# Kernel optimization log

Measured on AMD Instinct MI355X. Metric: run time of the kernel, lower is better.

## Reference

```python
import jax, jax.numpy as jnp
import numpy as np

N_NODES = 2_000_000
N_EDGES = 32_000_000
N_GRAPHS = 256


def setup_inputs() -> dict:
    key = jax.random.key(0)
    k1, k2, k3 = jax.random.split(key, 3)
    probs = jax.random.uniform(k1, (N_NODES,), dtype=jnp.float32)
    edge_index = jax.random.randint(k2, (2, N_EDGES), 0, N_NODES, dtype=jnp.int64)
    batch = jnp.sort(jax.random.randint(k3, (N_NODES,), 0, N_GRAPHS, dtype=jnp.int64))
    penalty_coefficient = jnp.float32(0.25)
    return {
        "probs": probs,
        "edge_index": edge_index,
        "batch": batch,
        "penalty_coefficient": penalty_coefficient,
    }


def reference(probs, edge_index, batch, penalty_coefficient):
    # num_graphs = batch.max() + 1 (concrete; batch is a static index array)
    num_graphs = int(np.asarray(batch).max()) + 1

    row, col = edge_index[0], edge_index[1]
    # remove_self_loops: drop edges with row == col -> mask instead of filter (static shapes)
    not_self_loop = (row != col).astype(probs.dtype)

    # expected distance: sum over non-self-loop edges of (1 - p_u)(1 - p_v), / num_graphs
    vertex_row = probs[row]  # [E]
    vertex_col = probs[col]  # [E]
    expected_distance = jnp.sum((1.0 - vertex_row) * (1.0 - vertex_col) * not_self_loop) / num_graphs

    # per-graph sum of probs (the original's python loop over graphs == segment_sum)
    probs_sum = jax.ops.segment_sum(probs, batch, num_segments=num_graphs)  # [G]
    expected_weight = probs_sum.mean()

    loss = penalty_coefficient * expected_distance + expected_weight
    return jnp.stack([loss, expected_weight, expected_distance])
```

## Files before the change

### kernel.cpp

```cpp
#include <hip/hip_runtime.h>
#include <hip/hip_fp16.h>

#define THREADS 256

typedef int int4v __attribute__((ext_vector_type(4)));


__device__ __forceinline__ float h2f_bits(unsigned v) {
    __half_raw hr;
    hr.x = (unsigned short)v;
    return __half2float((__half)hr);
}

__device__ __forceinline__ void block_reduce_atomic(float local, double* dst,
                                                    double* sdata) {
    double d = (double)local;
    #pragma unroll
    for (int off = 32; off > 0; off >>= 1)
        d += __shfl_down(d, off, 64);
    int lane = threadIdx.x & 63;
    int wid  = threadIdx.x >> 6;
    if (lane == 0) sdata[wid] = d;
    __syncthreads();
    if (threadIdx.x == 0) {
        double s = 0.0;
        #pragma unroll
        for (int i = 0; i < (THREADS / 64); ++i) s += sdata[i];
        atomicAdd(dst, s);
    }
}

__global__ void __launch_bounds__(THREADS) build_table_kernel(
        const float* __restrict__ probs,
        unsigned short* __restrict__ qt,
        double* __restrict__ ws,
        long long n_nodes) {
    __shared__ double sdata[THREADS / 64];
    long long n4 = n_nodes >> 2;
    const float4* p4 = (const float4*)probs;
    ushort4* q4 = (ushort4*)qt;
    long long tid = (long long)blockIdx.x * blockDim.x + threadIdx.x;
    long long stride = (long long)gridDim.x * blockDim.x;

    if (tid == 0) qt[n_nodes] = (unsigned short)0;

    float local = 0.0f;
    for (long long i = tid; i < n4; i += stride) {
        float4 v = p4[i];
        local += (v.x + v.y) + (v.z + v.w);
        ushort4 q;
        q.x = __half_as_ushort(__float2half(1.0f - v.x));
        q.y = __half_as_ushort(__float2half(1.0f - v.y));
        q.z = __half_as_ushort(__float2half(1.0f - v.z));
        q.w = __half_as_ushort(__float2half(1.0f - v.w));
        q4[i] = q;
    }
    for (long long i = (n4 << 2) + tid; i < n_nodes; i += stride) {
        float p = probs[i];
        local += p;
        qt[i] = __half_as_ushort(__float2half(1.0f - p));
    }

    block_reduce_atomic(local, ws + 1, sdata);
}

__global__ void edge_sum_kernel(
        const unsigned short* __restrict__ qt,
        const int* __restrict__ row,
        const int* __restrict__ col,
        double* __restrict__ ws,
        long long n_edges,
        int sentinel) {
    __shared__ double sdata[THREADS / 64];
    long long n4 = n_edges >> 2;
    long long G4 = n4 >> 2;
    long long t  = (long long)blockIdx.x * blockDim.x + threadIdx.x;

    const int4v* row4 = (const int4v*)row;
    const int4v* col4 = (const int4v*)col;

    float local = 0.0f;
    if (t < G4) {
        unsigned av[16], bv[16];
        #pragma unroll
        for (int k = 0; k < 4; ++k) {
            int4v u = __builtin_nontemporal_load(&row4[t + (long long)k * G4]);
            int4v v = __builtin_nontemporal_load(&col4[t + (long long)k * G4]);
            int v0 = (u.x == v.x) ? sentinel : v.x;
            int v1 = (u.y == v.y) ? sentinel : v.y;
            int v2 = (u.z == v.z) ? sentinel : v.z;
            int v3 = (u.w == v.w) ? sentinel : v.w;
            av[4 * k + 0] = qt[u.x];
            av[4 * k + 1] = qt[u.y];
            av[4 * k + 2] = qt[u.z];
            av[4 * k + 3] = qt[u.w];
            bv[4 * k + 0] = qt[v0];
            bv[4 * k + 1] = qt[v1];
            bv[4 * k + 2] = qt[v2];
            bv[4 * k + 3] = qt[v3];
        }

        #pragma unroll
        for (int i = 0; i < 16; ++i)
            local += h2f_bits(av[i]) * h2f_bits(bv[i]);
    }

    long long covered = G4 << 4;
    long long total_threads = (long long)gridDim.x * blockDim.x;
    for (long long e = covered + t; e < n_edges; e += total_threads) {
        int uu = row[e], vv = col[e];
        int vr = (uu == vv) ? sentinel : vv;
        local += h2f_bits(qt[uu]) * h2f_bits(qt[vr]);
    }

    block_reduce_atomic(local, ws, sdata);
}

__global__ void finalize_kernel(const double* __restrict__ ws,
                                const int* __restrict__ batch,
                                long long n_nodes,
                                const float* __restrict__ pc,
                                float* __restrict__ out) {
    double edge_s = ws[0];
    double prob_s = ws[1];
    double G = (double)(batch[n_nodes - 1] + 1);
    double ed = edge_s / G;
    double ew = prob_s / G;
    double loss = (double)pc[0] * ed + ew;
    out[0] = (float)loss;
    out[1] = (float)ew;
    out[2] = (float)ed;
}

extern "C" void kernel_launch(void* const* d_in, const int* in_sizes, int n_in,
                              void* d_out, int out_size, void* d_ws, size_t ws_size,
                              hipStream_t stream) {
    const float* probs = (const float*)d_in[0];
    const int* edge_index = (const int*)d_in[1];
    const int* batch = (const int*)d_in[2];
    const float* pc = (const float*)d_in[3];

    long long n_nodes = (long long)in_sizes[0];
    long long n_edges = (long long)in_sizes[1] / 2;
    const int* row = edge_index;
    const int* col = edge_index + n_edges;

    double* ws = (double*)d_ws;
    hipMemsetAsync(ws, 0, 2 * sizeof(double), stream);

    unsigned short* qt = (unsigned short*)((char*)d_ws + 256);
    build_table_kernel<<<512, THREADS, 0, stream>>>(probs, qt, ws, n_nodes);

    long long T = (n_edges >> 2) >> 2;
    long long blocks = (T + THREADS - 1) / THREADS;
    if (blocks < 1) blocks = 1;
    edge_sum_kernel<<<(int)blocks, THREADS, 0, stream>>>(qt, row, col, ws,
                                                         n_edges, (int)n_nodes);

    finalize_kernel<<<1, 1, 0, stream>>>(ws, batch, n_nodes, pc, (float*)d_out);
}
```

Measured before the change: 319.0 us.

## Use one int4 edge chunk per thread with nontemporal inline-asm gathers

The edge kernel now gives each thread one 4-edge chunk instead of sixteen edges, which launches four times as many blocks. The half-precision table gathers are issued as inline-asm global_load_ushort with the nt cache hint, followed by an explicit waitcnt and a scheduling barrier. The intent is more parallelism for latency hiding and less cache pollution from the gathers. In exchange, the random gathers into the 4MB table may lose cache reuse, and more blocks mean more block reductions and double-precision atomics.

```diff
diff --git a/kernel.cpp b/kernel.cpp
--- a/kernel.cpp
+++ b/kernel.cpp
@@ -73,39 +73,51 @@
         int sentinel) {
     __shared__ double sdata[THREADS / 64];
     long long n4 = n_edges >> 2;
-    long long G4 = n4 >> 2;
     long long t  = (long long)blockIdx.x * blockDim.x + threadIdx.x;
 
     const int4v* row4 = (const int4v*)row;
     const int4v* col4 = (const int4v*)col;
 
     float local = 0.0f;
-    if (t < G4) {
-        unsigned av[16], bv[16];
-        #pragma unroll
-        for (int k = 0; k < 4; ++k) {
-            int4v u = __builtin_nontemporal_load(&row4[t + (long long)k * G4]);
-            int4v v = __builtin_nontemporal_load(&col4[t + (long long)k * G4]);
-            int v0 = (u.x == v.x) ? sentinel : v.x;
-            int v1 = (u.y == v.y) ? sentinel : v.y;
-            int v2 = (u.z == v.z) ? sentinel : v.z;
-            int v3 = (u.w == v.w) ? sentinel : v.w;
-            av[4 * k + 0] = qt[u.x];
-            av[4 * k + 1] = qt[u.y];
-            av[4 * k + 2] = qt[u.z];
-            av[4 * k + 3] = qt[u.w];
-            bv[4 * k + 0] = qt[v0];
-            bv[4 * k + 1] = qt[v1];
-            bv[4 * k + 2] = qt[v2];
-            bv[4 * k + 3] = qt[v3];
+    if (t < n4) {
+        int4v u = __builtin_nontemporal_load(&row4[t]);
+        int4v v = __builtin_nontemporal_load(&col4[t]);
+
+        int v0 = (u.x == v.x) ? sentinel : v.x;
+        int v1 = (u.y == v.y) ? sentinel : v.y;
+        int v2 = (u.z == v.z) ? sentinel : v.z;
+        int v3 = (u.w == v.w) ? sentinel : v.w;
+
+        unsigned long long base = (unsigned long long)qt;
+        unsigned a0, a1, a2, a3, b0, b1, b2, b3;
+        {
+            unsigned long long x0 = base + 2ull * (unsigned)u.x;
+            unsigned long long x1 = base + 2ull * (unsigned)u.y;
+            unsigned long long x2 = base + 2ull * (unsigned)u.z;
+            unsigned long long x3 = base + 2ull * (unsigned)u.w;
+            unsigned long long y0 = base + 2ull * (unsigned)v0;
+            unsigned long long y1 = base + 2ull * (unsigned)v1;
+            unsigned long long y2 = base + 2ull * (unsigned)v2;
+            unsigned long long y3 = base + 2ull * (unsigned)v3;
+            asm volatile("global_load_ushort %0, %1, off nt" : "=v"(a0) : "v"(x0));
+            asm volatile("global_load_ushort %0, %1, off nt" : "=v"(a1) : "v"(x1));
+            asm volatile("global_load_ushort %0, %1, off nt" : "=v"(a2) : "v"(x2));
+            asm volatile("global_load_ushort %0, %1, off nt" : "=v"(a3) : "v"(x3));
+            asm volatile("global_load_ushort %0, %1, off nt" : "=v"(b0) : "v"(y0));
+            asm volatile("global_load_ushort %0, %1, off nt" : "=v"(b1) : "v"(y1));
+            asm volatile("global_load_ushort %0, %1, off nt" : "=v"(b2) : "v"(y2));
+            asm volatile("global_load_ushort %0, %1, off nt" : "=v"(b3) : "v"(y3));
         }
+        asm volatile("s_waitcnt vmcnt(0)" ::: "memory");
+        __builtin_amdgcn_sched_barrier(0);
 
-        #pragma unroll
-        for (int i = 0; i < 16; ++i)
-            local += h2f_bits(av[i]) * h2f_bits(bv[i]);
+        local += h2f_bits(a0) * h2f_bits(b0);
+        local += h2f_bits(a1) * h2f_bits(b1);
+        local += h2f_bits(a2) * h2f_bits(b2);
+        local += h2f_bits(a3) * h2f_bits(b3);
     }
 
-    long long covered = G4 << 4;
+    long long covered = n4 << 2;
     long long total_threads = (long long)gridDim.x * blockDim.x;
     for (long long e = covered + t; e < n_edges; e += total_threads) {
         int uu = row[e], vv = col[e];
@@ -151,7 +163,7 @@
     unsigned short* qt = (unsigned short*)((char*)d_ws + 256);
     build_table_kernel<<<512, THREADS, 0, stream>>>(probs, qt, ws, n_nodes);
 
-    long long T = (n_edges >> 2) >> 2;
+    long long T = n_edges >> 2;
     long long blocks = (T + THREADS - 1) / THREADS;
     if (blocks < 1) blocks = 1;
     edge_sum_kernel<<<(int)blocks, THREADS, 0, stream>>>(qt, row, col, ws,
```

Result: slower. 669.8 us (+109.9%).
